# Optimization experiments

Measured on AMD Instinct MI355X. Metric: run time of the kernel, lower is better.

The kernel has to match this reference:

```python
import jax, jax.numpy as jnp
import numpy as np

N, E = 50000, 800000
D_IN, D_H, D_OUT = 128, 128, 128


def setup_inputs() -> dict:
    key = jax.random.key(0)
    ks = jax.random.split(key, 8)
    x = jax.random.normal(ks[0], (N, D_IN), dtype=jnp.float32)
    edge_index = jax.random.randint(ks[1], (2, E), 0, N, dtype=jnp.int64)
    s_in = 1.0 / np.sqrt(D_IN)
    s_h = 1.0 / np.sqrt(D_H)
    W1 = jax.random.normal(ks[2], (D_IN, D_H), dtype=jnp.float32) * s_in
    b1 = jnp.zeros((D_H,), jnp.float32)
    Wg = jax.random.normal(ks[3], (D_H, D_H), dtype=jnp.float32) * s_h
    bg = jnp.zeros((D_H,), jnp.float32)
    W2 = jax.random.normal(ks[4], (D_H, D_OUT), dtype=jnp.float32) * s_h
    b2 = jnp.zeros((D_OUT,), jnp.float32)
    return {"x": x, "edge_index": edge_index, "W1": W1, "b1": b1,
            "Wg": Wg, "bg": bg, "W2": W2, "b2": b2}


def reference(x, edge_index, W1, b1, Wg, bg, W2, b2):
    # Linear -> ReLU
    h = jax.nn.relu(x @ W1 + b1)                      # [N, D_H]
    # GCNConv: transform, add self-loops, sym-normalize, scatter-aggregate
    h = h @ Wg                                        # [N, D_H]
    row, col = edge_index[0], edge_index[1]
    loop = jnp.arange(N, dtype=edge_index.dtype)
    row = jnp.concatenate([row, loop])                # [E+N] sources
    col = jnp.concatenate([col, loop])                # [E+N] targets
    deg = jax.ops.segment_sum(jnp.ones(E + N, h.dtype), col, num_segments=N)
    dinv = jnp.where(deg > 0, jax.lax.rsqrt(deg), 0.0)
    norm = dinv[row] * dinv[col]                      # [E+N]
    agg = jax.ops.segment_sum(h[row] * norm[:, None], col, num_segments=N)
    agg = agg + bg                                    # GCNConv bias
    # ReLU -> Linear
    return jax.nn.relu(agg) @ W2 + b2                 # [N, D_OUT]
```

## Files before the change

kernel.cpp:

```cpp
#include <hip/hip_runtime.h>

#define D 128

typedef short bf16x8 __attribute__((ext_vector_type(8)));
typedef float f32x4 __attribute__((ext_vector_type(4)));

static __device__ __forceinline__ unsigned int f2bf(float f) {
  unsigned int u = __float_as_uint(f);
  return (u + 0x7FFFu + ((u >> 16) & 1u)) >> 16;
}
static __device__ __forceinline__ unsigned int pack2bf(float lo, float hi) {
  return f2bf(lo) | (f2bf(hi) << 16);
}
static __device__ __forceinline__ float bf_lo(unsigned int v) {
  return __uint_as_float(v << 16);
}
static __device__ __forceinline__ float bf_hi(unsigned int v) {
  return __uint_as_float(v & 0xFFFF0000u);
}


__global__ __launch_bounds__(256) void k_prep(const float* __restrict__ W1,
                                              const float* __restrict__ Wg,
                                              const float* __restrict__ W2,
                                              unsigned short* __restrict__ WT,
                                              int* __restrict__ deg, int N) {
  if (blockIdx.x < 3) {
    const float* W = (blockIdx.x == 0) ? W1 : (blockIdx.x == 1) ? Wg : W2;
    unsigned short* T = WT + blockIdx.x * 16384;
    for (int idx = threadIdx.x; idx < 16384; idx += 256) {
      int k = idx >> 7, j = idx & 127;
      T[j * 128 + k] = (unsigned short)f2bf(W[idx]);
    }
  } else {
    int i = (blockIdx.x - 3) * 256 + threadIdx.x;
    if (i < N) deg[i] = 0;
  }
}


#define FILL_CHUNK 2048

__global__ __launch_bounds__(256) void k_fill(const int* __restrict__ ei, int E,
                                              int* __restrict__ deg,
                                              unsigned short* __restrict__ csr16,
                                              int cap) {
  const int p = blockIdx.x & 7;
  const int base = (blockIdx.x >> 3) * FILL_CHUNK;
  const int t = threadIdx.x;
  int c[8];
#pragma unroll
  for (int u = 0; u < 8; ++u) {
    int e = base + u * 256 + t;
    c[u] = (e < E) ? ei[E + e] : -1;
  }
#pragma unroll
  for (int u = 0; u < 8; ++u) {
    if (c[u] >= 0 && (c[u] & 7) == p) {
      int e = base + u * 256 + t;
      int r = ei[e];
      int pos = atomicAdd(&deg[c[u]], 1);
      if (pos < cap)
        csr16[(size_t)c[u] * cap + pos] = (unsigned short)r;
    }
  }
}


__global__ __launch_bounds__(256) void k_mlp(const float* __restrict__ x,
                                             const unsigned short* __restrict__ W1T,
                                             const float* __restrict__ b1,
                                             const unsigned short* __restrict__ WgT,
                                             const int* __restrict__ deg,
                                             unsigned short* __restrict__ h2, int N) {
  __shared__ unsigned short xs[64][136];
  __shared__ unsigned short wB[128][136];
  const int t = threadIdx.x;
  const int wave = t >> 6, lane = t & 63;
  const int rowBase = blockIdx.x * 64;
  const int ar = lane & 15, kg = lane >> 4;

#pragma unroll
  for (int i = 0; i < 8; ++i) {
    int idx = t + i * 256;
    int r = idx >> 5, c4 = (idx & 31) << 2;
    float4 v = make_float4(0.f, 0.f, 0.f, 0.f);
    int gr = rowBase + r;
    if (gr < N) v = *(const float4*)(x + (size_t)gr * D + c4);
    *(unsigned int*)&xs[r][c4]     = pack2bf(v.x, v.y);
    *(unsigned int*)&xs[r][c4 + 2] = pack2bf(v.z, v.w);
  }
#pragma unroll
  for (int i = 0; i < 8; ++i) {
    int idx = t + i * 256;
    int r = idx >> 4, c8 = (idx & 15) << 3;
    *(uint4*)&wB[r][c8] = *(const uint4*)(W1T + r * 128 + c8);
  }
  __syncthreads();

  float bias1[8];
#pragma unroll
  for (int cf = 0; cf < 8; ++cf) bias1[cf] = b1[cf * 16 + ar];
  float dnv[4];
#pragma unroll
  for (int reg = 0; reg < 4; ++reg) {
    int gr = rowBase + wave * 16 + 4 * kg + reg;
    dnv[reg] = (gr < N) ? rsqrtf((float)(deg[gr] + 1)) : 0.f;
  }

  f32x4 acc[8];
#pragma unroll
  for (int cf = 0; cf < 8; ++cf) acc[cf] = (f32x4){0.f, 0.f, 0.f, 0.f};
#pragma unroll
  for (int ks = 0; ks < 4; ++ks) {
    bf16x8 a = *(const bf16x8*)&xs[wave * 16 + ar][ks * 32 + kg * 8];
#pragma unroll
    for (int cf = 0; cf < 8; ++cf) {
      bf16x8 b = *(const bf16x8*)&wB[cf * 16 + ar][ks * 32 + kg * 8];
      acc[cf] = __builtin_amdgcn_mfma_f32_16x16x32_bf16(a, b, acc[cf], 0, 0, 0);
    }
  }

#pragma unroll
  for (int cf = 0; cf < 8; ++cf)
#pragma unroll
    for (int reg = 0; reg < 4; ++reg) {
      float v = fmaxf(acc[cf][reg] + bias1[cf], 0.f);
      xs[wave * 16 + 4 * kg + reg][cf * 16 + ar] = (unsigned short)f2bf(v);
    }
  __syncthreads();

#pragma unroll
  for (int i = 0; i < 8; ++i) {
    int idx = t + i * 256;
    int r = idx >> 4, c8 = (idx & 15) << 3;
    *(uint4*)&wB[r][c8] = *(const uint4*)(WgT + r * 128 + c8);
  }
  __syncthreads();

#pragma unroll
  for (int cf = 0; cf < 8; ++cf) acc[cf] = (f32x4){0.f, 0.f, 0.f, 0.f};
#pragma unroll
  for (int ks = 0; ks < 4; ++ks) {
    bf16x8 a = *(const bf16x8*)&xs[wave * 16 + ar][ks * 32 + kg * 8];
#pragma unroll
    for (int cf = 0; cf < 8; ++cf) {
      bf16x8 b = *(const bf16x8*)&wB[cf * 16 + ar][ks * 32 + kg * 8];
      acc[cf] = __builtin_amdgcn_mfma_f32_16x16x32_bf16(a, b, acc[cf], 0, 0, 0);
    }
  }

#pragma unroll
  for (int cf = 0; cf < 8; ++cf)
#pragma unroll
    for (int reg = 0; reg < 4; ++reg) {
      int gr = rowBase + wave * 16 + 4 * kg + reg;
      if (gr < N)
        h2[(size_t)gr * D + cf * 16 + ar] = (unsigned short)f2bf(acc[cf][reg] * dnv[reg]);
    }
}


__global__ __launch_bounds__(256) void k_agg(const unsigned short* __restrict__ h2,
                                             const int* __restrict__ deg,
                                             const unsigned short* __restrict__ csr16,
                                             const float* __restrict__ bg,
                                             unsigned short* __restrict__ h3, int N, int cap) {
  const int half = threadIdx.x >> 5;
  const int hl = threadIdx.x & 31;
  const int n = blockIdx.x * 8 + half;
  if (n >= N) return;
  const uint2* h2v = (const uint2*)h2;
  uint2 vself = h2v[(size_t)n * 32 + hl];
  int dg = deg[n];
  float4 bgv = ((const float4*)bg)[hl];
  float dn = rsqrtf((float)(dg + 1));
  float a0 = 0.f, a1 = 0.f, a2 = 0.f, a3 = 0.f;
  int cnt = min(dg, cap);
  size_t base = (size_t)n * cap;
  int i = 0;
  for (; i + 16 <= cnt; i += 16) {
    uint4 pa = *(const uint4*)(csr16 + base + i);
    uint4 pb = *(const uint4*)(csr16 + base + i + 8);
    int s[16] = {(int)(pa.x & 0xFFFFu), (int)(pa.x >> 16),
                 (int)(pa.y & 0xFFFFu), (int)(pa.y >> 16),
                 (int)(pa.z & 0xFFFFu), (int)(pa.z >> 16),
                 (int)(pa.w & 0xFFFFu), (int)(pa.w >> 16),
                 (int)(pb.x & 0xFFFFu), (int)(pb.x >> 16),
                 (int)(pb.y & 0xFFFFu), (int)(pb.y >> 16),
                 (int)(pb.z & 0xFFFFu), (int)(pb.z >> 16),
                 (int)(pb.w & 0xFFFFu), (int)(pb.w >> 16)};
    uint2 v[16];
#pragma unroll
    for (int u = 0; u < 16; ++u) v[u] = h2v[(size_t)s[u] * 32 + hl];
#pragma unroll
    for (int u = 0; u < 16; ++u) {
      a0 += bf_lo(v[u].x); a1 += bf_hi(v[u].x);
      a2 += bf_lo(v[u].y); a3 += bf_hi(v[u].y);
    }
  }
  for (; i + 8 <= cnt; i += 8) {
    uint4 pk = *(const uint4*)(csr16 + base + i);
    int s[8] = {(int)(pk.x & 0xFFFFu), (int)(pk.x >> 16),
                (int)(pk.y & 0xFFFFu), (int)(pk.y >> 16),
                (int)(pk.z & 0xFFFFu), (int)(pk.z >> 16),
                (int)(pk.w & 0xFFFFu), (int)(pk.w >> 16)};
    uint2 v[8];
#pragma unroll
    for (int u = 0; u < 8; ++u) v[u] = h2v[(size_t)s[u] * 32 + hl];
#pragma unroll
    for (int u = 0; u < 8; ++u) {
      a0 += bf_lo(v[u].x); a1 += bf_hi(v[u].x);
      a2 += bf_lo(v[u].y); a3 += bf_hi(v[u].y);
    }
  }
  for (; i < cnt; ++i) {
    int s = csr16[base + i];
    uint2 v = h2v[(size_t)s * 32 + hl];
    a0 += bf_lo(v.x); a1 += bf_hi(v.x);
    a2 += bf_lo(v.y); a3 += bf_hi(v.y);
  }
  a0 += bf_lo(vself.x); a1 += bf_hi(vself.x);
  a2 += bf_lo(vself.y); a3 += bf_hi(vself.y);
  float r0 = fmaxf(fmaf(a0, dn, bgv.x), 0.f);
  float r1 = fmaxf(fmaf(a1, dn, bgv.y), 0.f);
  float r2 = fmaxf(fmaf(a2, dn, bgv.z), 0.f);
  float r3 = fmaxf(fmaf(a3, dn, bgv.w), 0.f);
  uint2 o;
  o.x = pack2bf(r0, r1);
  o.y = pack2bf(r2, r3);
  ((uint2*)h3)[(size_t)n * 32 + hl] = o;
}


__global__ __launch_bounds__(256) void k_out(const unsigned short* __restrict__ h3,
                                             const unsigned short* __restrict__ W2T,
                                             const float* __restrict__ b2,
                                             float* __restrict__ out, int N) {
  __shared__ unsigned short xs[64][136];
  __shared__ unsigned short wB[128][136];
  const int t = threadIdx.x;
  const int wave = t >> 6, lane = t & 63;
  const int rowBase = blockIdx.x * 64;
  const int ar = lane & 15, kg = lane >> 4;

#pragma unroll
  for (int i = 0; i < 4; ++i) {
    int idx = t + i * 256;
    int r = idx >> 4, c8 = (idx & 15) << 3;
    uint4 v = make_uint4(0u, 0u, 0u, 0u);
    int gr = rowBase + r;
    if (gr < N) v = *(const uint4*)(h3 + (size_t)gr * D + c8);
    *(uint4*)&xs[r][c8] = v;
  }
#pragma unroll
  for (int i = 0; i < 8; ++i) {
    int idx = t + i * 256;
    int r = idx >> 4, c8 = (idx & 15) << 3;
    *(uint4*)&wB[r][c8] = *(const uint4*)(W2T + r * 128 + c8);
  }
  __syncthreads();

  float bias2[8];
#pragma unroll
  for (int cf = 0; cf < 8; ++cf) bias2[cf] = b2[cf * 16 + ar];

  f32x4 acc[8];
#pragma unroll
  for (int cf = 0; cf < 8; ++cf) acc[cf] = (f32x4){0.f, 0.f, 0.f, 0.f};
#pragma unroll
  for (int ks = 0; ks < 4; ++ks) {
    bf16x8 a8 = *(const bf16x8*)&xs[wave * 16 + ar][ks * 32 + kg * 8];
#pragma unroll
    for (int cf = 0; cf < 8; ++cf) {
      bf16x8 b8 = *(const bf16x8*)&wB[cf * 16 + ar][ks * 32 + kg * 8];
      acc[cf] = __builtin_amdgcn_mfma_f32_16x16x32_bf16(a8, b8, acc[cf], 0, 0, 0);
    }
  }

#pragma unroll
  for (int cf = 0; cf < 8; ++cf)
#pragma unroll
    for (int reg = 0; reg < 4; ++reg) {
      int gr = rowBase + wave * 16 + 4 * kg + reg;
      if (gr < N)
        out[(size_t)gr * D + cf * 16 + ar] = acc[cf][reg] + bias2[cf];
    }
}


extern "C" void kernel_launch(void* const* d_in, const int* in_sizes, int n_in,
                              void* d_out, int out_size, void* d_ws, size_t ws_size,
                              hipStream_t stream) {
  const float* x  = (const float*)d_in[0];
  const int*   ei = (const int*)d_in[1];
  const float* W1 = (const float*)d_in[2];
  const float* b1 = (const float*)d_in[3];
  const float* Wg = (const float*)d_in[4];
  const float* bg = (const float*)d_in[5];
  const float* W2 = (const float*)d_in[6];
  const float* b2 = (const float*)d_in[7];
  const int N = in_sizes[0] / D;
  const int E = in_sizes[1] / 2;
  float* out = (float*)d_out;

  unsigned short* h2 = (unsigned short*)d_ws;
  unsigned short* h3 = h2 + (size_t)N * D;
  unsigned short* WT = h3 + (size_t)N * D;
  int*   deg  = (int*)(WT + 3 * 16384);
  unsigned short* csr16 = (unsigned short*)(deg + N);

  size_t fixed = (size_t)N * D * 4 + 3 * 16384 * 2 + (size_t)N * 4;
  int cap;
  if (ws_size >= fixed + (size_t)N * 64 * 2)      cap = 64;
  else if (ws_size >= fixed + (size_t)N * 48 * 2) cap = 48;
  else return;

  const int nzb = (N + 255) / 256;
  const int fillb = ((E + FILL_CHUNK - 1) / FILL_CHUNK) * 8;

  k_prep<<<3 + nzb, 256, 0, stream>>>(W1, Wg, W2, WT, deg, N);
  k_fill<<<fillb, 256, 0, stream>>>(ei, E, deg, csr16, cap);
  k_mlp <<<(N + 63) / 64, 256, 0, stream>>>(x, WT, b1, WT + 16384, deg, h2, N);
  k_agg <<<(N + 7) / 8, 256, 0, stream>>>(h2, deg, csr16, bg, h3, N, cap);
  k_out <<<(N + 63) / 64, 256, 0, stream>>>(h3, WT + 2 * 16384, b2, out, N);
}
```

Measured before the change: 125.8 us.

## Merge CSR fill and MLP into one interleaved launch, move degree norm to aggregation

Combines the edge-fill kernel and the two-layer MLP kernel into one launch whose blocks are interleaved in groups of 32 fill blocks and 8 MLP blocks, so the atomic-bound scatter and the MFMA work can overlap. The MLP no longer depends on degrees, so the source-side normalisation moves into the aggregation, which now reads deg[s] per neighbour and applies rsqrt weights. The MLP also drops the LDS staging of weights and reads B fragments straight from global memory. The tradeoff is extra random deg loads and rsqrt work in the gather, plus uncached global weight reads in the MFMA loop.

```diff
diff --git a/kernel.cpp b/kernel.cpp
--- a/kernel.cpp
+++ b/kernel.cpp
@@ -1,6 +1,8 @@
 #include <hip/hip_runtime.h>
 
 #define D 128
+#define FILL_CHUNK 2048
+#define SG 40
 
 typedef short bf16x8 __attribute__((ext_vector_type(8)));
 typedef float f32x4 __attribute__((ext_vector_type(4)));
@@ -39,45 +41,48 @@
 }
 
 
-#define FILL_CHUNK 2048
-
-__global__ __launch_bounds__(256) void k_fill(const int* __restrict__ ei, int E,
-                                              int* __restrict__ deg,
-                                              unsigned short* __restrict__ csr16,
-                                              int cap) {
-  const int p = blockIdx.x & 7;
-  const int base = (blockIdx.x >> 3) * FILL_CHUNK;
+__global__ __launch_bounds__(256, 4) void k_merged(const int* __restrict__ ei, int E,
+                                                   int* __restrict__ deg,
+                                                   unsigned short* __restrict__ csr16, int cap,
+                                                   const float* __restrict__ x,
+                                                   const unsigned short* __restrict__ W1T,
+                                                   const float* __restrict__ b1,
+                                                   const unsigned short* __restrict__ WgT,
+                                                   unsigned short* __restrict__ h2, int N,
+                                                   int FILLU, int MLPU) {
+  __shared__ unsigned short xs[64][136];
+  const int sg = blockIdx.x / SG;
+  const int j = blockIdx.x % SG;
   const int t = threadIdx.x;
-  int c[8];
-#pragma unroll
-  for (int u = 0; u < 8; ++u) {
-    int e = base + u * 256 + t;
-    c[u] = (e < E) ? ei[E + e] : -1;
-  }
-#pragma unroll
-  for (int u = 0; u < 8; ++u) {
-    if (c[u] >= 0 && (c[u] & 7) == p) {
+
+  if (j < 32) {
+    const int u0 = sg * 32 + j;
+    if (u0 >= FILLU) return;
+    const int p = u0 & 7;
+    const int base = (u0 >> 3) * FILL_CHUNK;
+    int c[8];
+#pragma unroll
+    for (int u = 0; u < 8; ++u) {
       int e = base + u * 256 + t;
-      int r = ei[e];
-      int pos = atomicAdd(&deg[c[u]], 1);
-      if (pos < cap)
-        csr16[(size_t)c[u] * cap + pos] = (unsigned short)r;
-    }
-  }
-}
-
-
-__global__ __launch_bounds__(256) void k_mlp(const float* __restrict__ x,
-                                             const unsigned short* __restrict__ W1T,
-                                             const float* __restrict__ b1,
-                                             const unsigned short* __restrict__ WgT,
-                                             const int* __restrict__ deg,
-                                             unsigned short* __restrict__ h2, int N) {
-  __shared__ unsigned short xs[64][136];
-  __shared__ unsigned short wB[128][136];
-  const int t = threadIdx.x;
+      c[u] = (e < E) ? ei[E + e] : -1;
+    }
+#pragma unroll
+    for (int u = 0; u < 8; ++u) {
+      if (c[u] >= 0 && (c[u] & 7) == p) {
+        int e = base + u * 256 + t;
+        int r = ei[e];
+        int pos = atomicAdd(&deg[c[u]], 1);
+        if (pos < cap)
+          csr16[(size_t)c[u] * cap + pos] = (unsigned short)r;
+      }
+    }
+    return;
+  }
+
+  const int m = sg * 8 + (j - 32);
+  if (m >= MLPU) return;
   const int wave = t >> 6, lane = t & 63;
-  const int rowBase = blockIdx.x * 64;
+  const int rowBase = m * 64;
   const int ar = lane & 15, kg = lane >> 4;
 
 #pragma unroll
@@ -90,23 +95,11 @@
     *(unsigned int*)&xs[r][c4]     = pack2bf(v.x, v.y);
     *(unsigned int*)&xs[r][c4 + 2] = pack2bf(v.z, v.w);
   }
-#pragma unroll
-  for (int i = 0; i < 8; ++i) {
-    int idx = t + i * 256;
-    int r = idx >> 4, c8 = (idx & 15) << 3;
-    *(uint4*)&wB[r][c8] = *(const uint4*)(W1T + r * 128 + c8);
-  }
   __syncthreads();
 
   float bias1[8];
 #pragma unroll
   for (int cf = 0; cf < 8; ++cf) bias1[cf] = b1[cf * 16 + ar];
-  float dnv[4];
-#pragma unroll
-  for (int reg = 0; reg < 4; ++reg) {
-    int gr = rowBase + wave * 16 + 4 * kg + reg;
-    dnv[reg] = (gr < N) ? rsqrtf((float)(deg[gr] + 1)) : 0.f;
-  }
 
   f32x4 acc[8];
 #pragma unroll
@@ -116,7 +109,7 @@
     bf16x8 a = *(const bf16x8*)&xs[wave * 16 + ar][ks * 32 + kg * 8];
 #pragma unroll
     for (int cf = 0; cf < 8; ++cf) {
-      bf16x8 b = *(const bf16x8*)&wB[cf * 16 + ar][ks * 32 + kg * 8];
+      bf16x8 b = *(const bf16x8*)(W1T + (cf * 16 + ar) * 128 + ks * 32 + kg * 8);
       acc[cf] = __builtin_amdgcn_mfma_f32_16x16x32_bf16(a, b, acc[cf], 0, 0, 0);
     }
   }
@@ -128,15 +121,6 @@
       float v = fmaxf(acc[cf][reg] + bias1[cf], 0.f);
       xs[wave * 16 + 4 * kg + reg][cf * 16 + ar] = (unsigned short)f2bf(v);
     }
-  __syncthreads();
-
-#pragma unroll
-  for (int i = 0; i < 8; ++i) {
-    int idx = t + i * 256;
-    int r = idx >> 4, c8 = (idx & 15) << 3;
-    *(uint4*)&wB[r][c8] = *(const uint4*)(WgT + r * 128 + c8);
-  }
-  __syncthreads();
 
 #pragma unroll
   for (int cf = 0; cf < 8; ++cf) acc[cf] = (f32x4){0.f, 0.f, 0.f, 0.f};
@@ -145,7 +129,7 @@
     bf16x8 a = *(const bf16x8*)&xs[wave * 16 + ar][ks * 32 + kg * 8];
 #pragma unroll
     for (int cf = 0; cf < 8; ++cf) {
-      bf16x8 b = *(const bf16x8*)&wB[cf * 16 + ar][ks * 32 + kg * 8];
+      bf16x8 b = *(const bf16x8*)(WgT + (cf * 16 + ar) * 128 + ks * 32 + kg * 8);
       acc[cf] = __builtin_amdgcn_mfma_f32_16x16x32_bf16(a, b, acc[cf], 0, 0, 0);
     }
   }
@@ -156,7 +140,7 @@
     for (int reg = 0; reg < 4; ++reg) {
       int gr = rowBase + wave * 16 + 4 * kg + reg;
       if (gr < N)
-        h2[(size_t)gr * D + cf * 16 + ar] = (unsigned short)f2bf(acc[cf][reg] * dnv[reg]);
+        h2[(size_t)gr * D + cf * 16 + ar] = (unsigned short)f2bf(acc[cf][reg]);
     }
 }
 
@@ -190,13 +174,17 @@
                  (int)(pb.y & 0xFFFFu), (int)(pb.y >> 16),
                  (int)(pb.z & 0xFFFFu), (int)(pb.z >> 16),
                  (int)(pb.w & 0xFFFFu), (int)(pb.w >> 16)};
+    int dgs[16];
+#pragma unroll
+    for (int u = 0; u < 16; ++u) dgs[u] = deg[s[u]];
     uint2 v[16];
 #pragma unroll
     for (int u = 0; u < 16; ++u) v[u] = h2v[(size_t)s[u] * 32 + hl];
 #pragma unroll
     for (int u = 0; u < 16; ++u) {
-      a0 += bf_lo(v[u].x); a1 += bf_hi(v[u].x);
-      a2 += bf_lo(v[u].y); a3 += bf_hi(v[u].y);
+      float w = rsqrtf((float)(dgs[u] + 1));
+      a0 = fmaf(w, bf_lo(v[u].x), a0); a1 = fmaf(w, bf_hi(v[u].x), a1);
+      a2 = fmaf(w, bf_lo(v[u].y), a2); a3 = fmaf(w, bf_hi(v[u].y), a3);
     }
   }
   for (; i + 8 <= cnt; i += 8) {
@@ -205,23 +193,28 @@
                 (int)(pk.y & 0xFFFFu), (int)(pk.y >> 16),
                 (int)(pk.z & 0xFFFFu), (int)(pk.z >> 16),
                 (int)(pk.w & 0xFFFFu), (int)(pk.w >> 16)};
+    int dgs[8];
+#pragma unroll
+    for (int u = 0; u < 8; ++u) dgs[u] = deg[s[u]];
     uint2 v[8];
 #pragma unroll
     for (int u = 0; u < 8; ++u) v[u] = h2v[(size_t)s[u] * 32 + hl];
 #pragma unroll
     for (int u = 0; u < 8; ++u) {
-      a0 += bf_lo(v[u].x); a1 += bf_hi(v[u].x);
-      a2 += bf_lo(v[u].y); a3 += bf_hi(v[u].y);
+      float w = rsqrtf((float)(dgs[u] + 1));
+      a0 = fmaf(w, bf_lo(v[u].x), a0); a1 = fmaf(w, bf_hi(v[u].x), a1);
+      a2 = fmaf(w, bf_lo(v[u].y), a2); a3 = fmaf(w, bf_hi(v[u].y), a3);
     }
   }
   for (; i < cnt; ++i) {
     int s = csr16[base + i];
+    float w = rsqrtf((float)(deg[s] + 1));
     uint2 v = h2v[(size_t)s * 32 + hl];
-    a0 += bf_lo(v.x); a1 += bf_hi(v.x);
-    a2 += bf_lo(v.y); a3 += bf_hi(v.y);
-  }
-  a0 += bf_lo(vself.x); a1 += bf_hi(vself.x);
-  a2 += bf_lo(vself.y); a3 += bf_hi(vself.y);
+    a0 = fmaf(w, bf_lo(v.x), a0); a1 = fmaf(w, bf_hi(v.x), a1);
+    a2 = fmaf(w, bf_lo(v.y), a2); a3 = fmaf(w, bf_hi(v.y), a3);
+  }
+  a0 = fmaf(dn, bf_lo(vself.x), a0); a1 = fmaf(dn, bf_hi(vself.x), a1);
+  a2 = fmaf(dn, bf_lo(vself.y), a2); a3 = fmaf(dn, bf_hi(vself.y), a3);
   float r0 = fmaxf(fmaf(a0, dn, bgv.x), 0.f);
   float r1 = fmaxf(fmaf(a1, dn, bgv.y), 0.f);
   float r2 = fmaxf(fmaf(a2, dn, bgv.z), 0.f);
@@ -317,11 +310,14 @@
   else return;
 
   const int nzb = (N + 255) / 256;
-  const int fillb = ((E + FILL_CHUNK - 1) / FILL_CHUNK) * 8;
-
-  k_prep<<<3 + nzb, 256, 0, stream>>>(W1, Wg, W2, WT, deg, N);
-  k_fill<<<fillb, 256, 0, stream>>>(ei, E, deg, csr16, cap);
-  k_mlp <<<(N + 63) / 64, 256, 0, stream>>>(x, WT, b1, WT + 16384, deg, h2, N);
-  k_agg <<<(N + 7) / 8, 256, 0, stream>>>(h2, deg, csr16, bg, h3, N, cap);
-  k_out <<<(N + 63) / 64, 256, 0, stream>>>(h3, WT + 2 * 16384, b2, out, N);
-}
+  const int FILLU = ((E + FILL_CHUNK - 1) / FILL_CHUNK) * 8;
+  const int MLPU  = (N + 63) / 64;
+  int nsg = (FILLU + 31) / 32;
+  if ((MLPU + 7) / 8 > nsg) nsg = (MLPU + 7) / 8;
+
+  k_prep  <<<3 + nzb, 256, 0, stream>>>(W1, Wg, W2, WT, deg, N);
+  k_merged<<<nsg * SG, 256, 0, stream>>>(ei, E, deg, csr16, cap,
+                                         x, WT, b1, WT + 16384, h2, N, FILLU, MLPU);
+  k_agg   <<<(N + 7) / 8, 256, 0, stream>>>(h2, deg, csr16, bg, h3, N, cap);
+  k_out   <<<(N + 63) / 64, 256, 0, stream>>>(h3, WT + 2 * 16384, b2, out, N);
+}
```

Result: slower. 149.4 us (+18.7%).

## Fuse neighbor aggregation with output linear layer in one kernel

Applied to the files above, without the earlier changes.

Merges the aggregation kernel and the output GEMM so each 64-row block gathers neighbor sums into shared memory and then runs the MFMA output projection directly. This removes the h3 intermediate write and readback plus one kernel launch. The W2 operand is now read straight from global memory (cached) instead of being staged in LDS. The trade-off is fewer blocks (64 rows each instead of 8) for the latency-bound gather, which may reduce the parallelism available to hide memory latency.

```diff
diff --git a/kernel.cpp b/kernel.cpp
--- a/kernel.cpp
+++ b/kernel.cpp
@@ -1,6 +1,7 @@
 #include <hip/hip_runtime.h>
 
 #define D 128
+#define FILL_CHUNK 2048
 
 typedef short bf16x8 __attribute__((ext_vector_type(8)));
 typedef float f32x4 __attribute__((ext_vector_type(4)));
@@ -38,8 +39,6 @@
   }
 }
 
-
-#define FILL_CHUNK 2048
 
 __global__ __launch_bounds__(256) void k_fill(const int* __restrict__ ei, int E,
                                               int* __restrict__ deg,
@@ -161,106 +160,90 @@
 }
 
 
-__global__ __launch_bounds__(256) void k_agg(const unsigned short* __restrict__ h2,
-                                             const int* __restrict__ deg,
-                                             const unsigned short* __restrict__ csr16,
-                                             const float* __restrict__ bg,
-                                             unsigned short* __restrict__ h3, int N, int cap) {
-  const int half = threadIdx.x >> 5;
-  const int hl = threadIdx.x & 31;
-  const int n = blockIdx.x * 8 + half;
-  if (n >= N) return;
+__global__ __launch_bounds__(256) void k_aggout(const unsigned short* __restrict__ h2,
+                                                const int* __restrict__ deg,
+                                                const unsigned short* __restrict__ csr16,
+                                                const float* __restrict__ bg,
+                                                const unsigned short* __restrict__ W2T,
+                                                const float* __restrict__ b2,
+                                                float* __restrict__ out, int N, int cap) {
+  __shared__ unsigned short xs[64][136];
+  const int t = threadIdx.x;
+  const int half = t >> 5;
+  const int hl = t & 31;
+  const int rowBase = blockIdx.x * 64;
   const uint2* h2v = (const uint2*)h2;
-  uint2 vself = h2v[(size_t)n * 32 + hl];
-  int dg = deg[n];
   float4 bgv = ((const float4*)bg)[hl];
-  float dn = rsqrtf((float)(dg + 1));
-  float a0 = 0.f, a1 = 0.f, a2 = 0.f, a3 = 0.f;
-  int cnt = min(dg, cap);
-  size_t base = (size_t)n * cap;
-  int i = 0;
-  for (; i + 16 <= cnt; i += 16) {
-    uint4 pa = *(const uint4*)(csr16 + base + i);
-    uint4 pb = *(const uint4*)(csr16 + base + i + 8);
-    int s[16] = {(int)(pa.x & 0xFFFFu), (int)(pa.x >> 16),
-                 (int)(pa.y & 0xFFFFu), (int)(pa.y >> 16),
-                 (int)(pa.z & 0xFFFFu), (int)(pa.z >> 16),
-                 (int)(pa.w & 0xFFFFu), (int)(pa.w >> 16),
-                 (int)(pb.x & 0xFFFFu), (int)(pb.x >> 16),
-                 (int)(pb.y & 0xFFFFu), (int)(pb.y >> 16),
-                 (int)(pb.z & 0xFFFFu), (int)(pb.z >> 16),
-                 (int)(pb.w & 0xFFFFu), (int)(pb.w >> 16)};
-    uint2 v[16];
-#pragma unroll
-    for (int u = 0; u < 16; ++u) v[u] = h2v[(size_t)s[u] * 32 + hl];
-#pragma unroll
-    for (int u = 0; u < 16; ++u) {
-      a0 += bf_lo(v[u].x); a1 += bf_hi(v[u].x);
-      a2 += bf_lo(v[u].y); a3 += bf_hi(v[u].y);
-    }
-  }
-  for (; i + 8 <= cnt; i += 8) {
-    uint4 pk = *(const uint4*)(csr16 + base + i);
-    int s[8] = {(int)(pk.x & 0xFFFFu), (int)(pk.x >> 16),
-                (int)(pk.y & 0xFFFFu), (int)(pk.y >> 16),
-                (int)(pk.z & 0xFFFFu), (int)(pk.z >> 16),
-                (int)(pk.w & 0xFFFFu), (int)(pk.w >> 16)};
-    uint2 v[8];
-#pragma unroll
-    for (int u = 0; u < 8; ++u) v[u] = h2v[(size_t)s[u] * 32 + hl];
-#pragma unroll
-    for (int u = 0; u < 8; ++u) {
-      a0 += bf_lo(v[u].x); a1 += bf_hi(v[u].x);
-      a2 += bf_lo(v[u].y); a3 += bf_hi(v[u].y);
-    }
-  }
-  for (; i < cnt; ++i) {
-    int s = csr16[base + i];
-    uint2 v = h2v[(size_t)s * 32 + hl];
-    a0 += bf_lo(v.x); a1 += bf_hi(v.x);
-    a2 += bf_lo(v.y); a3 += bf_hi(v.y);
-  }
-  a0 += bf_lo(vself.x); a1 += bf_hi(vself.x);
-  a2 += bf_lo(vself.y); a3 += bf_hi(vself.y);
-  float r0 = fmaxf(fmaf(a0, dn, bgv.x), 0.f);
-  float r1 = fmaxf(fmaf(a1, dn, bgv.y), 0.f);
-  float r2 = fmaxf(fmaf(a2, dn, bgv.z), 0.f);
-  float r3 = fmaxf(fmaf(a3, dn, bgv.w), 0.f);
-  uint2 o;
-  o.x = pack2bf(r0, r1);
-  o.y = pack2bf(r2, r3);
-  ((uint2*)h3)[(size_t)n * 32 + hl] = o;
-}
-
-
-__global__ __launch_bounds__(256) void k_out(const unsigned short* __restrict__ h3,
-                                             const unsigned short* __restrict__ W2T,
-                                             const float* __restrict__ b2,
-                                             float* __restrict__ out, int N) {
-  __shared__ unsigned short xs[64][136];
-  __shared__ unsigned short wB[128][136];
-  const int t = threadIdx.x;
+
+#pragma unroll 2
+  for (int it = 0; it < 8; ++it) {
+    const int row = it * 8 + half;
+    const int n = rowBase + row;
+    uint2 o = make_uint2(0u, 0u);
+    if (n < N) {
+      uint2 vself = h2v[(size_t)n * 32 + hl];
+      int dg = deg[n];
+      float dn = rsqrtf((float)(dg + 1));
+      float a0 = 0.f, a1 = 0.f, a2 = 0.f, a3 = 0.f;
+      int cnt = min(dg, cap);
+      size_t base = (size_t)n * cap;
+      int i = 0;
+      for (; i + 16 <= cnt; i += 16) {
+        uint4 pa = *(const uint4*)(csr16 + base + i);
+        uint4 pb = *(const uint4*)(csr16 + base + i + 8);
+        int s[16] = {(int)(pa.x & 0xFFFFu), (int)(pa.x >> 16),
+                     (int)(pa.y & 0xFFFFu), (int)(pa.y >> 16),
+                     (int)(pa.z & 0xFFFFu), (int)(pa.z >> 16),
+                     (int)(pa.w & 0xFFFFu), (int)(pa.w >> 16),
+                     (int)(pb.x & 0xFFFFu), (int)(pb.x >> 16),
+                     (int)(pb.y & 0xFFFFu), (int)(pb.y >> 16),
+                     (int)(pb.z & 0xFFFFu), (int)(pb.z >> 16),
+                     (int)(pb.w & 0xFFFFu), (int)(pb.w >> 16)};
+        uint2 v[16];
+#pragma unroll
+        for (int u = 0; u < 16; ++u) v[u] = h2v[(size_t)s[u] * 32 + hl];
+#pragma unroll
+        for (int u = 0; u < 16; ++u) {
+          a0 += bf_lo(v[u].x); a1 += bf_hi(v[u].x);
+          a2 += bf_lo(v[u].y); a3 += bf_hi(v[u].y);
+        }
+      }
+      for (; i + 8 <= cnt; i += 8) {
+        uint4 pk = *(const uint4*)(csr16 + base + i);
+        int s[8] = {(int)(pk.x & 0xFFFFu), (int)(pk.x >> 16),
+                    (int)(pk.y & 0xFFFFu), (int)(pk.y >> 16),
+                    (int)(pk.z & 0xFFFFu), (int)(pk.z >> 16),
+                    (int)(pk.w & 0xFFFFu), (int)(pk.w >> 16)};
+        uint2 v[8];
+#pragma unroll
+        for (int u = 0; u < 8; ++u) v[u] = h2v[(size_t)s[u] * 32 + hl];
+#pragma unroll
+        for (int u = 0; u < 8; ++u) {
+          a0 += bf_lo(v[u].x); a1 += bf_hi(v[u].x);
+          a2 += bf_lo(v[u].y); a3 += bf_hi(v[u].y);
+        }
+      }
+      for (; i < cnt; ++i) {
+        int s = csr16[base + i];
+        uint2 v = h2v[(size_t)s * 32 + hl];
+        a0 += bf_lo(v.x); a1 += bf_hi(v.x);
+        a2 += bf_lo(v.y); a3 += bf_hi(v.y);
+      }
+      a0 += bf_lo(vself.x); a1 += bf_hi(vself.x);
+      a2 += bf_lo(vself.y); a3 += bf_hi(vself.y);
+      float r0 = fmaxf(fmaf(a0, dn, bgv.x), 0.f);
+      float r1 = fmaxf(fmaf(a1, dn, bgv.y), 0.f);
+      float r2 = fmaxf(fmaf(a2, dn, bgv.z), 0.f);
+      float r3 = fmaxf(fmaf(a3, dn, bgv.w), 0.f);
+      o.x = pack2bf(r0, r1);
+      o.y = pack2bf(r2, r3);
+    }
+    *(uint2*)&xs[row][hl * 4] = o;
+  }
+  __syncthreads();
+
   const int wave = t >> 6, lane = t & 63;
-  const int rowBase = blockIdx.x * 64;
   const int ar = lane & 15, kg = lane >> 4;
-
-#pragma unroll
-  for (int i = 0; i < 4; ++i) {
-    int idx = t + i * 256;
-    int r = idx >> 4, c8 = (idx & 15) << 3;
-    uint4 v = make_uint4(0u, 0u, 0u, 0u);
-    int gr = rowBase + r;
-    if (gr < N) v = *(const uint4*)(h3 + (size_t)gr * D + c8);
-    *(uint4*)&xs[r][c8] = v;
-  }
-#pragma unroll
-  for (int i = 0; i < 8; ++i) {
-    int idx = t + i * 256;
-    int r = idx >> 4, c8 = (idx & 15) << 3;
-    *(uint4*)&wB[r][c8] = *(const uint4*)(W2T + r * 128 + c8);
-  }
-  __syncthreads();
-
   float bias2[8];
 #pragma unroll
   for (int cf = 0; cf < 8; ++cf) bias2[cf] = b2[cf * 16 + ar];
@@ -273,7 +256,7 @@
     bf16x8 a8 = *(const bf16x8*)&xs[wave * 16 + ar][ks * 32 + kg * 8];
 #pragma unroll
     for (int cf = 0; cf < 8; ++cf) {
-      bf16x8 b8 = *(const bf16x8*)&wB[cf * 16 + ar][ks * 32 + kg * 8];
+      bf16x8 b8 = *(const bf16x8*)(W2T + (cf * 16 + ar) * 128 + ks * 32 + kg * 8);
       acc[cf] = __builtin_amdgcn_mfma_f32_16x16x32_bf16(a8, b8, acc[cf], 0, 0, 0);
     }
   }
@@ -305,12 +288,11 @@
   float* out = (float*)d_out;
 
   unsigned short* h2 = (unsigned short*)d_ws;
-  unsigned short* h3 = h2 + (size_t)N * D;
-  unsigned short* WT = h3 + (size_t)N * D;
+  unsigned short* WT = h2 + (size_t)N * D;
   int*   deg  = (int*)(WT + 3 * 16384);
   unsigned short* csr16 = (unsigned short*)(deg + N);
 
-  size_t fixed = (size_t)N * D * 4 + 3 * 16384 * 2 + (size_t)N * 4;
+  size_t fixed = (size_t)N * D * 2 + 3 * 16384 * 2 + (size_t)N * 4;
   int cap;
   if (ws_size >= fixed + (size_t)N * 64 * 2)      cap = 64;
   else if (ws_size >= fixed + (size_t)N * 48 * 2) cap = 48;
@@ -319,9 +301,8 @@
   const int nzb = (N + 255) / 256;
   const int fillb = ((E + FILL_CHUNK - 1) / FILL_CHUNK) * 8;
 
-  k_prep<<<3 + nzb, 256, 0, stream>>>(W1, Wg, W2, WT, deg, N);
-  k_fill<<<fillb, 256, 0, stream>>>(ei, E, deg, csr16, cap);
-  k_mlp <<<(N + 63) / 64, 256, 0, stream>>>(x, WT, b1, WT + 16384, deg, h2, N);
-  k_agg <<<(N + 7) / 8, 256, 0, stream>>>(h2, deg, csr16, bg, h3, N, cap);
-  k_out <<<(N + 63) / 64, 256, 0, stream>>>(h3, WT + 2 * 16384, b2, out, N);
-}
+  k_prep  <<<3 + nzb, 256, 0, stream>>>(W1, Wg, W2, WT, deg, N);
+  k_fill  <<<fillb, 256, 0, stream>>>(ei, E, deg, csr16, cap);
+  k_mlp   <<<(N + 63) / 64, 256, 0, stream>>>(x, WT, b1, WT + 16384, deg, h2, N);
+  k_aggout<<<(N + 63) / 64, 256, 0, stream>>>(h2, deg, csr16, bg, WT + 2 * 16384, b2, out, N, cap);
+}
```

Measured after the change: 144.6 us. 14.9% more time.
